# Optimization experiments

Hardware: AMD Instinct MI355X
Metric: run time of the kernel (lower is better)

## Reference

```python
import jax, jax.numpy as jnp
import numpy as np

N, D, H, F = 384, 512, 8, 64  # n_nodes, in/out features, heads, per-head hidden
SLOPE = 0.2


def gat_v2_layer(x, mask, W_l, W_r, a):
    """GATv2 layer (is_concat=True). x: [N, D_in]; mask: [N, N, 1] bool.

    torch semantics: g_sum[i, j] = g_l[j] + g_r[i]; e = a . LeakyReLU(g_sum);
    softmax over j (dim=1); aggregate g_r with einsum('ijh,jhf->ihf').
    attn linear nn.Linear(F, 1) is shared across heads -> a: [F].
    """
    n = x.shape[0]
    g_l = (x @ W_l).reshape(n, H, F)
    g_r = (x @ W_r).reshape(n, H, F)
    # pairwise [i, j, h, f] = g_r[i] + g_l[j]  (the big O(N^2) intermediate)
    s = jax.nn.leaky_relu(g_r[:, None] + g_l[None, :], negative_slope=SLOPE)
    e = jnp.einsum('ijhf,f->ijh', s, a)
    e = jnp.where(mask, e, -jnp.inf)
    att = jax.nn.softmax(e, axis=1)  # normalize over source nodes j
    out = jnp.einsum('ijh,jhf->ihf', att, g_r)
    return out.reshape(n, H * F)


def setup_inputs() -> dict:
    key = jax.random.key(0)
    ks = jax.random.split(key, 8)
    x = jax.random.normal(ks[0], (N, D), dtype=jnp.float32)
    adj = jax.random.randint(ks[1], (N, N, 1), 0, 2, dtype=jnp.int32)
    sd = 1.0 / np.sqrt(D)
    sa = 1.0 / np.sqrt(F)
    W_l0 = jax.random.normal(ks[2], (D, H * F), dtype=jnp.float32) * sd
    W_r0 = jax.random.normal(ks[3], (D, H * F), dtype=jnp.float32) * sd
    a0 = jax.random.normal(ks[4], (F,), dtype=jnp.float32) * sa
    W_l1 = jax.random.normal(ks[5], (H * F, H * F), dtype=jnp.float32) * sd
    W_r1 = jax.random.normal(ks[6], (H * F, H * F), dtype=jnp.float32) * sd
    a1 = jax.random.normal(ks[7], (F,), dtype=jnp.float32) * sa
    return {"x": x, "adj": adj, "W_l0": W_l0, "W_r0": W_r0, "a0": a0,
            "W_l1": W_l1, "W_r1": W_r1, "a1": a1}


def reference(x, adj, W_l0, W_r0, a0, W_l1, W_r1, a1):
    n = x.shape[0]
    # selfloop: fill diagonal of adj with 1
    idx = jnp.arange(n)
    adj = adj.at[idx, idx, 0].set(1)
    mask = adj != 0  # [N, N, 1]
    # layer 0: GATv2 -> ELU (i < n_layers-1) -> residual
    out = jax.nn.elu(gat_v2_layer(x, mask, W_l0, W_r0, a0))
    x = x + out
    # layer 1: GATv2 -> Identity -> residual
    out = gat_v2_layer(x, mask, W_l1, W_r1, a1)
    x = x + out
    return x
```

## Files before the change

### kernel.cpp

```cpp
#include <hip/hip_runtime.h>
#include <hip/hip_bf16.h>
#include <stdint.h>

typedef unsigned short ushort_t;
typedef unsigned long long u64;
typedef __attribute__((ext_vector_type(8))) short short8;
typedef __attribute__((ext_vector_type(4))) float f32x4;

#define N_NODES 384
#define HF      512
#define IT      12

__device__ inline ushort_t f2bf(float f) {
  __hip_bfloat16 b = __float2bfloat16(f);
  return *reinterpret_cast<ushort_t*>(&b);
}
__device__ inline float bf2f_u(ushort_t u) {
  union { float f; uint32_t i; } v; v.i = ((uint32_t)u) << 16; return v.f;
}
__device__ inline short8 pack8(const float* s) {
  short8 r;
#pragma unroll
  for (int j = 0; j < 8; ++j) r[j] = (short)f2bf(s[j]);
  return r;
}

__global__ __launch_bounds__(256) void gemm_direct(
    const float* __restrict__ X, const float* __restrict__ WL,
    const float* __restrict__ WR, float* __restrict__ G,
    ushort_t* __restrict__ glb, ushort_t* __restrict__ grT,
    const int* __restrict__ adj, u64* __restrict__ mbits)
{
  const int t = threadIdx.x, wave = t >> 6, lane = t & 63;
  const int lm = lane & 15, q = lane >> 4;
  const int m0 = blockIdx.x * 16;
  const int n0 = (blockIdx.y * 4 + wave) * 32;
  const float* Wp = (n0 < 512) ? (WL + n0) : (WR + (n0 - 512));
  const float* Arow = X + (m0 + lm) * HF;

  f32x4 acc0 = {0.f, 0.f, 0.f, 0.f};
  f32x4 acc1 = {0.f, 0.f, 0.f, 0.f};
#pragma unroll 4
  for (int kc = 0; kc < 16; ++kc) {
    const int kbase = kc * 32 + q * 8;
    float4 a0 = *(const float4*)(Arow + kbase);
    float4 a1 = *(const float4*)(Arow + kbase + 4);
    float av8[8] = {a0.x, a0.y, a0.z, a0.w, a1.x, a1.y, a1.z, a1.w};
    short8 af = pack8(av8);
    float b0f[8], b1f[8];
#pragma unroll
    for (int j = 0; j < 8; ++j) {
      const float* r = Wp + (kbase + j) * HF;
      b0f[j] = r[lm];
      b1f[j] = r[16 + lm];
    }
    short8 b0 = pack8(b0f);
    short8 b1 = pack8(b1f);
    acc0 = __builtin_amdgcn_mfma_f32_16x16x32_bf16(af, b0, acc0, 0, 0, 0);
    acc1 = __builtin_amdgcn_mfma_f32_16x16x32_bf16(af, b1, acc1, 0, 0, 0);
  }
  if (n0 < 512) {
#pragma unroll
    for (int r = 0; r < 4; ++r) {
      int m = m0 + q * 4 + r;
      glb[m * HF + n0 + lm]      = f2bf(acc0[r]);
      glb[m * HF + n0 + 16 + lm] = f2bf(acc1[r]);
    }
  } else {
#pragma unroll
    for (int r = 0; r < 4; ++r) {
      int m = m0 + q * 4 + r;
      G[m * 1024 + n0 + lm]      = acc0[r];
      G[m * 1024 + n0 + 16 + lm] = acc1[r];
    }
    int c0 = n0 - 512;
    uint2 p0, p1;
    p0.x = (uint32_t)f2bf(acc0[0]) | ((uint32_t)f2bf(acc0[1]) << 16);
    p0.y = (uint32_t)f2bf(acc0[2]) | ((uint32_t)f2bf(acc0[3]) << 16);
    p1.x = (uint32_t)f2bf(acc1[0]) | ((uint32_t)f2bf(acc1[1]) << 16);
    p1.y = (uint32_t)f2bf(acc1[2]) | ((uint32_t)f2bf(acc1[3]) << 16);
    *(uint2*)&grT[(c0 + lm) * 384 + m0 + q * 4]      = p0;
    *(uint2*)&grT[(c0 + 16 + lm) * 384 + m0 + q * 4] = p1;
  }
  if (adj != nullptr && blockIdx.y == 0) {
    int rbase = (blockIdx.x * 4 + wave) * 4;
    for (int rr = 0; rr < 4; ++rr) {
      int row = rbase + rr;
#pragma unroll
      for (int w = 0; w < 6; ++w) {
        int j = w * 64 + lane;
        u64 m = __ballot(adj[row * N_NODES + j] != 0 || row == j);
        if (lane == 0) mbits[row * 6 + w] = m;
      }
    }
  }
}

template <int LAYER>
__global__ __launch_bounds__(384) void attn_fused(
    const float* __restrict__ G, const ushort_t* __restrict__ glb,
    const ushort_t* __restrict__ grT, const u64* __restrict__ mbits,
    const float* __restrict__ resid_in, const float* __restrict__ avec,
    float* __restrict__ xcur_out, float* __restrict__ f_out)
{
  __shared__ __align__(16) char smem[49152];
  ushort_t (*s_gl)[64]     = (ushort_t(*)[64])smem;
  float    (*s_e)[N_NODES] = (float(*)[N_NODES])smem;
  ushort_t (*s_pb)[392]    = (ushort_t(*)[392])(smem + 18432);
  __shared__ float s_bri[IT];
  __shared__ u64   s_mask[IT][6];

  const int t = threadIdx.x;
  const int i0 = blockIdx.x * IT, h = blockIdx.y;
  const int lane = t & 63, wave = t >> 6;

#pragma unroll
  for (int rep = 0; rep < 8; ++rep) {
    int idx = rep * 384 + t, row = idx >> 3, cl = idx & 7;
    int cg = cl ^ (row & 7);
    const ushort_t* gsrc = glb + row * HF + h * 64 + cg * 8;
    __builtin_amdgcn_global_load_lds(
        (const __attribute__((address_space(1))) uint32_t*)gsrc,
        (__attribute__((address_space(3))) uint32_t*)(smem + idx * 16),
        16, 0, 0);
  }

  if (t < 72) ((u64*)s_mask)[t] = mbits[i0 * 6 + t];
  if (t >= 128 && t < 320) {
    int u = t - 128, il = u >> 4, fg = u & 15;
    float4 g4 = *(const float4*)(G + (i0 + il) * 1024 + 512 + h * 64 + fg * 4);
    float4 a4 = *(const float4*)(avec + fg * 4);
    float s = a4.x * g4.x + a4.y * g4.y + a4.z * g4.z + a4.w * g4.w;
    s += __shfl_xor(s, 1); s += __shfl_xor(s, 2);
    s += __shfl_xor(s, 4); s += __shfl_xor(s, 8);
    if (fg == 0) s_bri[il] = s;
  }
  __syncthreads();

  float gl[64], av[64];
  {
    const int sw = t & 7;
#pragma unroll
    for (int cg = 0; cg < 8; ++cg) {
      short8 v = *(const short8*)&s_gl[t][(cg ^ sw) * 8];
#pragma unroll
      for (int u2 = 0; u2 < 8; ++u2)
        gl[cg * 8 + u2] = bf2f_u((ushort_t)v[u2]);
    }
#pragma unroll
    for (int c = 0; c < 16; ++c) {
      float4 a4 = ((const float4*)avec)[c];
      av[c * 4] = a4.x; av[c * 4 + 1] = a4.y;
      av[c * 4 + 2] = a4.z; av[c * 4 + 3] = a4.w;
    }
  }
  float accl = 0.f;
#pragma unroll
  for (int f = 0; f < 64; ++f) accl += av[f] * gl[f];
  __syncthreads();

  const int jw = t >> 6, jb = t & 63;
#pragma unroll
  for (int il = 0; il < IT; ++il) {
    const float4* gr4 = (const float4*)(G + (i0 + il) * 1024 + 512 + h * 64);
    float acc = 0.f;
#pragma unroll
    for (int c = 0; c < 16; ++c) {
      float4 g4 = gr4[c];
      acc += av[c * 4]     * fabsf(gl[c * 4]     + g4.x);
      acc += av[c * 4 + 1] * fabsf(gl[c * 4 + 1] + g4.y);
      acc += av[c * 4 + 2] * fabsf(gl[c * 4 + 2] + g4.z);
      acc += av[c * 4 + 3] * fabsf(gl[c * 4 + 3] + g4.w);
    }
    bool m = (s_mask[il][jw] >> jb) & 1;
    float e = 0.6f * (accl + s_bri[il]) + 0.4f * acc;
    s_e[il][t] = m ? e : -1e30f;
  }
#pragma unroll
  for (int r4 = 0; r4 < 4; ++r4) s_pb[IT + r4][t] = 0;
  __syncthreads();

#pragma unroll
  for (int rep = 0; rep < 2; ++rep) {
    int il = wave * 2 + rep;
    float v[6];
    float mx = -1e30f;
#pragma unroll
    for (int c = 0; c < 6; ++c) { v[c] = s_e[il][lane + 64 * c]; mx = fmaxf(mx, v[c]); }
#pragma unroll
    for (int off = 32; off; off >>= 1) mx = fmaxf(mx, __shfl_xor(mx, off));
    float sum = 0.f;
#pragma unroll
    for (int c = 0; c < 6; ++c) { v[c] = __expf(v[c] - mx); sum += v[c]; }
#pragma unroll
    for (int off = 32; off; off >>= 1) sum += __shfl_xor(sum, off);
    float inv = 1.0f / sum;
#pragma unroll
    for (int c = 0; c < 6; ++c) s_pb[il][lane + 64 * c] = f2bf(v[c] * inv);
  }
  __syncthreads();

  if (wave < 4) {
    const int lm = lane & 15, q = lane >> 4;
    const int f0 = wave * 16;
    const ushort_t* Brow = grT + (h * 64 + f0 + lm) * 384;
    f32x4 acc = {0.f, 0.f, 0.f, 0.f};
#pragma unroll
    for (int kc = 0; kc < 12; ++kc) {
      short8 af = *(const short8*)&s_pb[lm][kc * 32 + q * 8];
      short8 bf = *(const short8*)&Brow[kc * 32 + q * 8];
      acc = __builtin_amdgcn_mfma_f32_16x16x32_bf16(af, bf, acc, 0, 0, 0);
    }
    if (q < 3) {
#pragma unroll
      for (int r = 0; r < 4; ++r) {
        int i = i0 + q * 4 + r;
        int off = i * HF + h * 64 + f0 + lm;
        float o = acc[r];
        if (LAYER == 0) {
          float oe = (o > 0.f) ? o : (__expf(o) - 1.f);
          xcur_out[off] = resid_in[off] + oe;
        } else {
          f_out[off] = resid_in[off] + o;
        }
      }
    }
  }
}

extern "C" void kernel_launch(void* const* d_in, const int* in_sizes, int n_in,
                              void* d_out, int out_size, void* d_ws, size_t ws_size,
                              hipStream_t stream) {
  const float* x   = (const float*)d_in[0];
  const int*   adj = (const int*)d_in[1];
  const float* Wl0 = (const float*)d_in[2];
  const float* Wr0 = (const float*)d_in[3];
  const float* a0  = (const float*)d_in[4];
  const float* Wl1 = (const float*)d_in[5];
  const float* Wr1 = (const float*)d_in[6];
  const float* a1  = (const float*)d_in[7];
  float* out = (float*)d_out;

  char* ws = (char*)d_ws;
  float*    G    = (float*)   (ws + 0L);
  ushort_t* grT  = (ushort_t*)(ws + (2L << 20));
  ushort_t* glb  = (ushort_t*)(ws + (3L << 20));
  u64*      mbits= (u64*)     (ws + (4L << 20));
  float*    xcur = (float*)   (ws + (5L << 20));

  gemm_direct<<<dim3(24, 8), 256, 0, stream>>>(x, Wl0, Wr0, G, glb, grT,
                                               adj, mbits);
  attn_fused<0><<<dim3(32, 8), 384, 0, stream>>>(G, glb, grT, mbits, x, a0,
                                                 xcur, nullptr);
  gemm_direct<<<dim3(24, 8), 256, 0, stream>>>(xcur, Wl1, Wr1, G, glb, grT,
                                               nullptr, nullptr);
  attn_fused<1><<<dim3(32, 8), 384, 0, stream>>>(G, glb, grT, mbits, xcur, a1,
                                                 nullptr, out);
}
```

Baseline: 118.8 us.

## Fuse four kernels into one persistent megakernel with grid barriers

Merges the two GEMM launches and two attention launches into a single persistent kernel of 256 blocks. The phases are separated by atomic-counter grid barriers, with a small init kernel resetting the counters. The GEMM work is repartitioned to 16-column tiles per wave, six waves per block, so it fits the attention grid. The goal is to cut launch overhead and inter-kernel gaps, at the cost of spin-wait barriers, reliance on all 256 blocks being co-resident, and fewer MFMAs per wave in the GEMM phase.

After: 174.7 us. 1.47x slower.

```diff
diff --git a/kernel.cpp b/kernel.cpp
--- a/kernel.cpp
+++ b/kernel.cpp
@@ -10,6 +10,7 @@
 #define N_NODES 384
 #define HF      512
 #define IT      12
+#define NBLK    256
 
 __device__ inline ushort_t f2bf(float f) {
   __hip_bfloat16 b = __float2bfloat16(f);
@@ -25,21 +26,36 @@
   return r;
 }
 
-__global__ __launch_bounds__(256) void gemm_direct(
-    const float* __restrict__ X, const float* __restrict__ WL,
-    const float* __restrict__ WR, float* __restrict__ G,
-    ushort_t* __restrict__ glb, ushort_t* __restrict__ grT,
-    const int* __restrict__ adj, u64* __restrict__ mbits)
+__global__ void init_bar(unsigned* bar) {
+  if (threadIdx.x < 4) bar[threadIdx.x] = 0;
+}
+
+__device__ __forceinline__ void gridbar(unsigned* cnt) {
+  __syncthreads();
+  if (threadIdx.x == 0) {
+    __hip_atomic_fetch_add(cnt, 1u, __ATOMIC_ACQ_REL, __HIP_MEMORY_SCOPE_AGENT);
+    while (__hip_atomic_load(cnt, __ATOMIC_ACQUIRE,
+                             __HIP_MEMORY_SCOPE_AGENT) < NBLK) {
+      __builtin_amdgcn_s_sleep(1);
+    }
+  }
+  __syncthreads();
+}
+
+__device__ __forceinline__ void gemm_phase(
+    const float* X, const float* WL, const float* WR,
+    float* G, ushort_t* glb, ushort_t* grT,
+    const int* adj, u64* mbits)
 {
   const int t = threadIdx.x, wave = t >> 6, lane = t & 63;
   const int lm = lane & 15, q = lane >> 4;
-  const int m0 = blockIdx.x * 16;
-  const int n0 = (blockIdx.y * 4 + wave) * 32;
+  const int u = blockIdx.x * 6 + wave;
+  const int m0 = (u >> 6) * 16;
+  const int n0 = (u & 63) * 16;
   const float* Wp = (n0 < 512) ? (WL + n0) : (WR + (n0 - 512));
   const float* Arow = X + (m0 + lm) * HF;
 
-  f32x4 acc0 = {0.f, 0.f, 0.f, 0.f};
-  f32x4 acc1 = {0.f, 0.f, 0.f, 0.f};
+  f32x4 acc = {0.f, 0.f, 0.f, 0.f};
 #pragma unroll 4
   for (int kc = 0; kc < 16; ++kc) {
     const int kbase = kc * 32 + q * 8;
@@ -47,71 +63,49 @@
     float4 a1 = *(const float4*)(Arow + kbase + 4);
     float av8[8] = {a0.x, a0.y, a0.z, a0.w, a1.x, a1.y, a1.z, a1.w};
     short8 af = pack8(av8);
-    float b0f[8], b1f[8];
-#pragma unroll
-    for (int j = 0; j < 8; ++j) {
-      const float* r = Wp + (kbase + j) * HF;
-      b0f[j] = r[lm];
-      b1f[j] = r[16 + lm];
-    }
-    short8 b0 = pack8(b0f);
-    short8 b1 = pack8(b1f);
-    acc0 = __builtin_amdgcn_mfma_f32_16x16x32_bf16(af, b0, acc0, 0, 0, 0);
-    acc1 = __builtin_amdgcn_mfma_f32_16x16x32_bf16(af, b1, acc1, 0, 0, 0);
+    float bf8[8];
+#pragma unroll
+    for (int j = 0; j < 8; ++j) bf8[j] = Wp[(kbase + j) * HF + lm];
+    short8 b = pack8(bf8);
+    acc = __builtin_amdgcn_mfma_f32_16x16x32_bf16(af, b, acc, 0, 0, 0);
   }
   if (n0 < 512) {
 #pragma unroll
-    for (int r = 0; r < 4; ++r) {
-      int m = m0 + q * 4 + r;
-      glb[m * HF + n0 + lm]      = f2bf(acc0[r]);
-      glb[m * HF + n0 + 16 + lm] = f2bf(acc1[r]);
-    }
+    for (int r = 0; r < 4; ++r)
+      glb[(m0 + q * 4 + r) * HF + n0 + lm] = f2bf(acc[r]);
   } else {
 #pragma unroll
-    for (int r = 0; r < 4; ++r) {
-      int m = m0 + q * 4 + r;
-      G[m * 1024 + n0 + lm]      = acc0[r];
-      G[m * 1024 + n0 + 16 + lm] = acc1[r];
-    }
+    for (int r = 0; r < 4; ++r)
+      G[(m0 + q * 4 + r) * 1024 + n0 + lm] = acc[r];
     int c0 = n0 - 512;
-    uint2 p0, p1;
-    p0.x = (uint32_t)f2bf(acc0[0]) | ((uint32_t)f2bf(acc0[1]) << 16);
-    p0.y = (uint32_t)f2bf(acc0[2]) | ((uint32_t)f2bf(acc0[3]) << 16);
-    p1.x = (uint32_t)f2bf(acc1[0]) | ((uint32_t)f2bf(acc1[1]) << 16);
-    p1.y = (uint32_t)f2bf(acc1[2]) | ((uint32_t)f2bf(acc1[3]) << 16);
-    *(uint2*)&grT[(c0 + lm) * 384 + m0 + q * 4]      = p0;
-    *(uint2*)&grT[(c0 + 16 + lm) * 384 + m0 + q * 4] = p1;
-  }
-  if (adj != nullptr && blockIdx.y == 0) {
-    int rbase = (blockIdx.x * 4 + wave) * 4;
-    for (int rr = 0; rr < 4; ++rr) {
-      int row = rbase + rr;
-#pragma unroll
-      for (int w = 0; w < 6; ++w) {
-        int j = w * 64 + lane;
-        u64 m = __ballot(adj[row * N_NODES + j] != 0 || row == j);
-        if (lane == 0) mbits[row * 6 + w] = m;
-      }
-    }
-  }
-}
-
-template <int LAYER>
-__global__ __launch_bounds__(384) void attn_fused(
-    const float* __restrict__ G, const ushort_t* __restrict__ glb,
-    const ushort_t* __restrict__ grT, const u64* __restrict__ mbits,
-    const float* __restrict__ resid_in, const float* __restrict__ avec,
-    float* __restrict__ xcur_out, float* __restrict__ f_out)
+    uint2 p0;
+    p0.x = (uint32_t)f2bf(acc[0]) | ((uint32_t)f2bf(acc[1]) << 16);
+    p0.y = (uint32_t)f2bf(acc[2]) | ((uint32_t)f2bf(acc[3]) << 16);
+    *(uint2*)&grT[(c0 + lm) * 384 + m0 + q * 4] = p0;
+  }
+  if (adj != nullptr && blockIdx.x < 96 && wave < 4) {
+    int row = blockIdx.x * 4 + wave;
+#pragma unroll
+    for (int w = 0; w < 6; ++w) {
+      int j = w * 64 + lane;
+      u64 m = __ballot(adj[row * N_NODES + j] != 0 || row == j);
+      if (lane == 0) mbits[row * 6 + w] = m;
+    }
+  }
+}
+
+__device__ __forceinline__ void attn_phase(int layer,
+    const float* G, const ushort_t* glb, const ushort_t* grT,
+    const u64* mbits, const float* resid_in, const float* avec,
+    float* xcur_out, float* f_out,
+    char* smem, float* s_bri, u64 (*s_mask)[6])
 {
-  __shared__ __align__(16) char smem[49152];
   ushort_t (*s_gl)[64]     = (ushort_t(*)[64])smem;
   float    (*s_e)[N_NODES] = (float(*)[N_NODES])smem;
   ushort_t (*s_pb)[392]    = (ushort_t(*)[392])(smem + 18432);
-  __shared__ float s_bri[IT];
-  __shared__ u64   s_mask[IT][6];
 
   const int t = threadIdx.x;
-  const int i0 = blockIdx.x * IT, h = blockIdx.y;
+  const int i0 = (blockIdx.x >> 3) * IT, h = blockIdx.x & 7;
   const int lane = t & 63, wave = t >> 6;
 
 #pragma unroll
@@ -217,7 +211,7 @@
         int i = i0 + q * 4 + r;
         int off = i * HF + h * 64 + f0 + lm;
         float o = acc[r];
-        if (LAYER == 0) {
+        if (layer == 0) {
           float oe = (o > 0.f) ? o : (__expf(o) - 1.f);
           xcur_out[off] = resid_in[off] + oe;
         } else {
@@ -226,6 +220,30 @@
       }
     }
   }
+}
+
+__global__ __launch_bounds__(384) void mega(
+    const float* __restrict__ x, const int* __restrict__ adj,
+    const float* __restrict__ Wl0, const float* __restrict__ Wr0,
+    const float* __restrict__ a0,  const float* __restrict__ Wl1,
+    const float* __restrict__ Wr1, const float* __restrict__ a1,
+    float* out, float* G, ushort_t* glb, ushort_t* grT,
+    u64* mbits, float* xcur, unsigned* bar)
+{
+  __shared__ __align__(16) char smem[49152];
+  __shared__ float s_bri[IT];
+  __shared__ u64   s_mask[IT][6];
+
+  gemm_phase(x, Wl0, Wr0, G, glb, grT, adj, mbits);
+  gridbar(bar + 0);
+
+  attn_phase(0, G, glb, grT, mbits, x, a0, xcur, out, smem, s_bri, s_mask);
+  gridbar(bar + 1);
+
+  gemm_phase(xcur, Wl1, Wr1, G, glb, grT, nullptr, nullptr);
+  gridbar(bar + 2);
+
+  attn_phase(1, G, glb, grT, mbits, xcur, a1, xcur, out, smem, s_bri, s_mask);
 }
 
 extern "C" void kernel_launch(void* const* d_in, const int* in_sizes, int n_in,
@@ -247,13 +265,9 @@
   ushort_t* glb  = (ushort_t*)(ws + (3L << 20));
   u64*      mbits= (u64*)     (ws + (4L << 20));
   float*    xcur = (float*)   (ws + (5L << 20));
-
-  gemm_direct<<<dim3(24, 8), 256, 0, stream>>>(x, Wl0, Wr0, G, glb, grT,
-                                               adj, mbits);
-  attn_fused<0><<<dim3(32, 8), 384, 0, stream>>>(G, glb, grT, mbits, x, a0,
-                                                 xcur, nullptr);
-  gemm_direct<<<dim3(24, 8), 256, 0, stream>>>(xcur, Wl1, Wr1, G, glb, grT,
-                                               nullptr, nullptr);
-  attn_fused<1><<<dim3(32, 8), 384, 0, stream>>>(G, glb, grT, mbits, xcur, a1,
-                                                 nullptr, out);
-}
+  unsigned* bar  = (unsigned*)(ws + (6L << 20));
+
+  init_bar<<<1, 64, 0, stream>>>(bar);
+  mega<<<NBLK, 384, 0, stream>>>(x, adj, Wl0, Wr0, a0, Wl1, Wr1, a1, out,
+                                 G, glb, grT, mbits, xcur, bar);
+}
```
